# Kernel optimization log

Hardware: AMD Instinct MI355X
Metric: run time of the kernel (lower is better)

## Reference

```python
import jax, jax.numpy as jnp
import numpy as np

NEG = -1e10
EPS = 1e-5
H = 4  # num_heads


def layer_norm(y, g, b):
    m = jnp.mean(y, axis=-1, keepdims=True)
    v = jnp.mean((y - m) ** 2, axis=-1, keepdims=True)
    return (y - m) * jax.lax.rsqrt(v + EPS) * g + b


def setup_inputs() -> dict:
    key = jax.random.key(0)
    B, N, C = 16, 1024, 256
    ks = jax.random.split(key, 12)
    std = 0.1  # matches trunc_normal_(std=0.1) init
    inp = {
        "x": jax.random.normal(ks[0], (B, N, C), jnp.float32),
        "K": jax.random.normal(ks[1], (B, N, N), jnp.float32),
        "n1": jax.random.randint(ks[2], (B,), 8, 33),
        "n2": jax.random.randint(ks[3], (B,), 8, 33),
        "qkv_w": jax.random.normal(ks[4], (3 * C, C), jnp.float32) * std,
        "qkv_b": jnp.zeros((3 * C,), jnp.float32),
        "proj_w": jax.random.normal(ks[5], (C, C), jnp.float32) * std,
        "proj_b": jnp.zeros((C,), jnp.float32),
        "ln1_g": jnp.ones((C,), jnp.float32),
        "ln1_b": jnp.zeros((C,), jnp.float32),
        "ln2_g": jnp.ones((C,), jnp.float32),
        "ln2_b": jnp.zeros((C,), jnp.float32),
        "fc1_w": jax.random.normal(ks[6], (4 * C, C), jnp.float32) * std,
        "fc1_b": jnp.zeros((4 * C,), jnp.float32),
        "fc2_w": jax.random.normal(ks[7], (C, 4 * C), jnp.float32) * std,
        "fc2_b": jnp.zeros((C,), jnp.float32),
    }
    return inp


def reference(x, K, n1, n2, qkv_w, qkv_b, proj_w, proj_b,
              ln1_g, ln1_b, ln2_g, ln2_b, fc1_w, fc1_b, fc2_w, fc2_b):
    B, N, C = x.shape
    D = C // H
    scale = D ** -0.5

    # --- attention block ---
    h = layer_norm(x, ln1_g, ln1_b)
    qkv = (h @ qkv_w.T + qkv_b).reshape(B, N, 3, H, D)
    qkv = jnp.transpose(qkv, (2, 0, 3, 1, 4))  # [3,B,H,N,D]
    q, k, v = qkv[0], qkv[1], qkv[2]

    attn = jnp.einsum('bhnd,bhmd->bhnm', q, k) * scale  # [B,H,N,N]

    # per-sample dynamic block mask: rows>=n1*n2 fully masked; cols>=n1*n2 masked
    nrc = (n1 * n2)[:, None]                  # [B,1]
    invalid = jnp.arange(N)[None, :] >= nrc   # [B,N]
    mask = invalid[:, :, None] | invalid[:, None, :]  # [B,N,N]
    attn = jnp.where(mask[:, None], NEG, attn)
    attn = attn + K[:, None]                  # broadcast K over heads

    a = jax.nn.softmax(attn, axis=-1)
    o = jnp.einsum('bhnm,bhmd->bhnd', a, v)
    o = jnp.transpose(o, (0, 2, 1, 3)).reshape(B, N, C)
    x = x + (o @ proj_w.T + proj_b)

    # --- MLP block (exact GELU as torch nn.GELU) ---
    h2 = layer_norm(x, ln2_g, ln2_b)
    m = jax.nn.gelu(h2 @ fc1_w.T + fc1_b, approximate=False)
    m = m @ fc2_w.T + fc2_b
    return x + m
```

## Files before the change

### kernel.cpp

```cpp
#include <hip/hip_runtime.h>
#include <math.h>
#include <stdint.h>

constexpr int Bc = 16, Nn = 1024, Cc = 256, Hh = 4;
constexpr int Mrows = Bc * Nn;
constexpr float EPSV = 1e-5f;

typedef __attribute__((ext_vector_type(4))) float f32x4;
typedef __attribute__((ext_vector_type(8))) short bf16x8;

__device__ inline float wave_reduce_sum(float v) {
#pragma unroll
  for (int m = 32; m >= 1; m >>= 1) v += __shfl_xor(v, m);
  return v;
}

__device__ inline short f2bf(float f) {
  uint32_t u = __builtin_bit_cast(uint32_t, f);
  u = (u + 0x7fffu + ((u >> 16) & 1u)) >> 16;
  return (short)u;
}
__device__ inline float bf2f(short s) {
  uint32_t u = ((uint32_t)(uint16_t)s) << 16;
  return __builtin_bit_cast(float, u);
}

__device__ inline float gelu_fast(float x) {
  float x2 = x * x;
  float u = x * (0.7978845608028654f + 0.0356774081f * x2);
  float e = __builtin_amdgcn_exp2f(u * 2.8853900817779268f);
  return x * (1.f - __builtin_amdgcn_rcpf(e + 1.f));
}

#define GLDS(gptr, lptr)                                             \
  __builtin_amdgcn_global_load_lds(                                  \
      (const __attribute__((address_space(1))) void*)(gptr),         \
      (__attribute__((address_space(3))) void*)(lptr), 16, 0, 0)

__global__ __launch_bounds__(256)
void cvt_all(const float* __restrict__ s0, short* __restrict__ d0,
             const float* __restrict__ s1, short* __restrict__ d1,
             const float* __restrict__ s2, short* __restrict__ d2,
             const float* __restrict__ s3, short* __restrict__ d3) {
  int bid = blockIdx.x;
  const float* s;
  short* d;
  int base;
  if (bid < 192)      { s = s0; d = d0; base = bid; }
  else if (bid < 256) { s = s1; d = d1; base = bid - 192; }
  else if (bid < 512) { s = s2; d = d2; base = bid - 256; }
  else                { s = s3; d = d3; base = bid - 512; }
  int i = (base * 256 + threadIdx.x) * 4;
  float4 v = *(const float4*)(s + i);
  short4 o;
  o.x = f2bf(v.x); o.y = f2bf(v.y); o.z = f2bf(v.z); o.w = f2bf(v.w);
  *(short4*)(d + i) = o;
}

__global__ __launch_bounds__(256)
void ln_kernel(const float* __restrict__ x, const float* __restrict__ g,
               const float* __restrict__ b, short* __restrict__ h) {
  int row = blockIdx.x * 4 + (threadIdx.x >> 6);
  int lane = threadIdx.x & 63;
  const float4* xr = (const float4*)(x + (size_t)row * Cc);
  float4 v = xr[lane];
  float s = v.x + v.y + v.z + v.w;
  float sq = v.x * v.x + v.y * v.y + v.z * v.z + v.w * v.w;
  s = wave_reduce_sum(s);
  sq = wave_reduce_sum(sq);
  float mean = s * (1.f / Cc);
  float var = sq * (1.f / Cc) - mean * mean;
  float inv = rsqrtf(var + EPSV);
  float4 gg = ((const float4*)g)[lane];
  float4 bb = ((const float4*)b)[lane];
  short4 o;
  o.x = f2bf((v.x - mean) * inv * gg.x + bb.x);
  o.y = f2bf((v.y - mean) * inv * gg.y + bb.y);
  o.z = f2bf((v.z - mean) * inv * gg.z + bb.z);
  o.w = f2bf((v.w - mean) * inv * gg.w + bb.w);
  *(short4*)(h + (size_t)row * Cc + lane * 4) = o;
}

__global__ __launch_bounds__(256)
void qkv_mfma(const short* __restrict__ A, const short* __restrict__ Bw,
              const float* __restrict__ bias, short* __restrict__ qkp,
              short* __restrict__ vtp) {
  __shared__ __align__(16) short As[2][128 * 64];
  __shared__ __align__(16) short Bs[2][128 * 64];
  int t = threadIdx.x;
  int w = t >> 6, lane = t & 63;
  int wm = w >> 1, wn = w & 1;
  int l16 = lane & 15, lhi = lane >> 4;
  int m0 = blockIdx.y * 128, n0 = blockIdx.x * 128;
  const bool vblk = (n0 >= 512);
  f32x4 acc[4][4] = {};

#pragma unroll
  for (int i = 0; i < 4; ++i) {
    int cc = i * 256 + t;
    int r = cc >> 3, sl = cc & 7, ssl = sl ^ (r & 7);
    GLDS(A + (size_t)(m0 + r) * 256 + ssl * 8, &As[0][cc * 8]);
    GLDS(Bw + (size_t)(n0 + r) * 256 + ssl * 8, &Bs[0][cc * 8]);
  }

  int cur = 0;
  for (int k0 = 0; k0 < 256; k0 += 64, cur ^= 1) {
    asm volatile("s_waitcnt vmcnt(0)" ::: "memory");
    __syncthreads();
    int kn = k0 + 64;
    if (kn < 256) {
      int nxt = cur ^ 1;
#pragma unroll
      for (int i = 0; i < 4; ++i) {
        int cc = i * 256 + t;
        int r = cc >> 3, sl = cc & 7, ssl = sl ^ (r & 7);
        GLDS(A + (size_t)(m0 + r) * 256 + kn + ssl * 8, &As[nxt][cc * 8]);
        GLDS(Bw + (size_t)(n0 + r) * 256 + kn + ssl * 8, &Bs[nxt][cc * 8]);
      }
    }
#pragma unroll
    for (int ks = 0; ks < 2; ++ks) {
      bf16x8 af[4], bg[4];
#pragma unroll
      for (int mi = 0; mi < 4; ++mi) {
        int row = wm * 64 + mi * 16 + l16;
        af[mi] = *(const bf16x8*)&As[cur][row * 64 + ((ks * 32 + lhi * 8) ^ ((row & 7) << 3))];
      }
#pragma unroll
      for (int ni = 0; ni < 4; ++ni) {
        int row = wn * 64 + ni * 16 + l16;
        bg[ni] = *(const bf16x8*)&Bs[cur][row * 64 + ((ks * 32 + lhi * 8) ^ ((row & 7) << 3))];
      }
      if (!vblk) {
#pragma unroll
        for (int mi = 0; mi < 4; ++mi)
#pragma unroll
          for (int ni = 0; ni < 4; ++ni)
            acc[mi][ni] = __builtin_amdgcn_mfma_f32_16x16x32_bf16(
                af[mi], bg[ni], acc[mi][ni], 0, 0, 0);
      } else {
#pragma unroll
        for (int mi = 0; mi < 4; ++mi)
#pragma unroll
          for (int ni = 0; ni < 4; ++ni)
            acc[mi][ni] = __builtin_amdgcn_mfma_f32_16x16x32_bf16(
                bg[ni], af[mi], acc[mi][ni], 0, 0, 0);
      }
    }
  }

  if (!vblk) {
    const bool isq = (n0 < 256);
#pragma unroll
    for (int mi = 0; mi < 4; ++mi) {
      int mbase = m0 + wm * 64 + mi * 16 + lhi * 4;
#pragma unroll
      for (int ni = 0; ni < 4; ++ni) {
        int n = n0 + wn * 64 + ni * 16 + l16;
        int s = n >> 8, hh = (n >> 6) & 3, d = n & 63;
        float bv = bias[n];
#pragma unroll
        for (int r = 0; r < 4; ++r) {
          int m = mbase + r;
          int b = m >> 10, rw = m & 1023;
          float v = acc[mi][ni][r] + bv;
          if (isq) v *= 0.125f;
          qkp[(size_t)s * 4194304 + (((size_t)(b * 4 + hh)) * 1024 + rw) * 64 + d] = f2bf(v);
        }
      }
    }
  } else {
#pragma unroll
    for (int mi = 0; mi < 4; ++mi) {
#pragma unroll
      for (int ni = 0; ni < 4; ++ni) {
#pragma unroll
        for (int r = 0; r < 4; ++r) {
          int n = n0 + wn * 64 + ni * 16 + lhi * 4 + r;
          int hh = (n >> 6) & 3, d = n & 63;
          int m = m0 + wm * 64 + mi * 16 + l16;
          int b = m >> 10, rw = m & 1023;
          float v = acc[mi][ni][r] + bias[n];
          vtp[(((size_t)(b * 4 + hh)) * 64 + d) * 1024 + rw] = f2bf(v);
        }
      }
    }
  }
}

__global__ __launch_bounds__(256)
void vmean_kernel(const short* __restrict__ vt, short* __restrict__ vmb) {
  __shared__ float part[64][4];
  int bh = blockIdx.x;
  int d = threadIdx.x >> 2, seg = threadIdx.x & 3;
  const short* p = vt + (size_t)bh * 65536 + (size_t)d * 1024 + seg * 256;
  float s = 0.f;
  for (int i = 0; i < 256; i += 8) {
    bf16x8 v = *(const bf16x8*)(p + i);
#pragma unroll
    for (int j = 0; j < 8; ++j) s += bf2f(v[j]);
  }
  part[d][seg] = s;
  __syncthreads();
  if (threadIdx.x < 64) {
    int dd = threadIdx.x;
    float tot = part[dd][0] + part[dd][1] + part[dd][2] + part[dd][3];
    vmb[bh * 64 + dd] = f2bf(tot * (1.f / 1024.f));
  }
}

__global__ __launch_bounds__(256)
void fattn_mfma(const short* __restrict__ qpk, const short* __restrict__ kpk,
                const short* __restrict__ vt, const float* __restrict__ Kmat,
                const int* __restrict__ n1, const int* __restrict__ n2,
                const short* __restrict__ vmb, short* __restrict__ o,
                float* __restrict__ pO, float* __restrict__ pL,
                int tiles_per_split) {
  int bh = blockIdx.y, b = bh >> 2, hh = bh & 3;
  int qt = blockIdx.x;
  int row0 = qt * 64;
  int sp = blockIdx.z;
  int nc = n1[b] * n2[b];
  int t = threadIdx.x;
  __shared__ short vms[64];
  if (t < 64) vms[t] = vmb[bh * 64 + t];
  __syncthreads();
  if (row0 >= nc) {
    if (sp == 0) {
      for (int idx = t; idx < 4096; idx += 256) {
        int r = idx >> 6, d = idx & 63;
        o[((size_t)(b * 1024 + row0 + r)) * 256 + hh * 64 + d] = vms[d];
      }
    }
    return;
  }
  int ntiles = (nc + 63) >> 6;
  int nsp = (ntiles + tiles_per_split - 1) / tiles_per_split;
  int jt0 = sp * tiles_per_split;
  if (jt0 >= ntiles) return;
  int jstart = jt0 * 64;
  int jend = min(jstart + tiles_per_split * 64, nc);
  const bool final_out = (nsp == 1);

  __shared__ __align__(16) short Ks[2][64 * 64];
  __shared__ __align__(16) short Vs[2][64 * 64];
  __shared__ __align__(16) short Ps[64 * 64];
  int w = t >> 6, lane = t & 63, l16 = lane & 15, lhi = lane >> 4;

  constexpr float LOG2E = 1.4426950408889634f;
  constexpr float MREF = 12.0f;

  const short* qb = qpk + (size_t)bh * 65536 + (size_t)(row0 + w * 16 + l16) * 64;
  bf16x8 qf0 = *(const bf16x8*)(qb + lhi * 8);
  bf16x8 qf1 = *(const bf16x8*)(qb + 32 + lhi * 8);

  f32x4 accO[4] = {};
  float lsum[4] = {};
  const float* Kb = Kmat + (size_t)b * 1048576 + (size_t)(row0 + w * 16) * 1024;

  f32x4 kvp[4];

#pragma unroll
  for (int i = 0; i < 2; ++i) {
    int cc = i * 256 + t;
    int r = cc >> 3, sl = cc & 7, ssl = sl ^ (r & 7);
    GLDS(kpk + (size_t)bh * 65536 + (size_t)(jstart + r) * 64 + ssl * 8, &Ks[0][cc * 8]);
    GLDS(vt + (size_t)bh * 65536 + (size_t)r * 1024 + jstart + ssl * 8, &Vs[0][cc * 8]);
  }
#pragma unroll
  for (int ni = 0; ni < 4; ++ni)
#pragma unroll
    for (int r = 0; r < 4; ++r)
      kvp[ni][r] =
          (Kb[(size_t)(lhi * 4 + r) * 1024 + jstart + ni * 16 + l16] - MREF) * LOG2E;

  int cur = 0;
  for (int j0 = jstart; j0 < jend; j0 += 64, cur ^= 1) {
    asm volatile("s_waitcnt vmcnt(0)" ::: "memory");
    __syncthreads();

    f32x4 kvc[4];
#pragma unroll
    for (int i = 0; i < 4; ++i) kvc[i] = kvp[i];
    int jn = j0 + 64;
    if (jn < jend) {
      int nxt = cur ^ 1;
#pragma unroll
      for (int i = 0; i < 2; ++i) {
        int cc = i * 256 + t;
        int r = cc >> 3, sl = cc & 7, ssl = sl ^ (r & 7);
        GLDS(kpk + (size_t)bh * 65536 + (size_t)(jn + r) * 64 + ssl * 8, &Ks[nxt][cc * 8]);
        GLDS(vt + (size_t)bh * 65536 + (size_t)r * 1024 + jn + ssl * 8, &Vs[nxt][cc * 8]);
      }
#pragma unroll
      for (int ni = 0; ni < 4; ++ni)
#pragma unroll
        for (int r = 0; r < 4; ++r)
          kvp[ni][r] =
              (Kb[(size_t)(lhi * 4 + r) * 1024 + jn + ni * 16 + l16] - MREF) * LOG2E;
    }

    f32x4 accS[4] = {};
#pragma unroll
    for (int ks = 0; ks < 2; ++ks) {
#pragma unroll
      for (int ni = 0; ni < 4; ++ni) {
        int row = ni * 16 + l16;
        bf16x8 kf = *(const bf16x8*)&Ks[cur][row * 64 + (((ks * 4 + lhi) ^ (row & 7)) << 3)];
        accS[ni] = __builtin_amdgcn_mfma_f32_16x16x32_bf16(
            ks ? qf1 : qf0, kf, accS[ni], 0, 0, 0);
      }
    }

#pragma unroll
    for (int ni = 0; ni < 4; ++ni) {
      bool valid = (j0 + ni * 16 + l16) < nc;
#pragma unroll
      for (int r = 0; r < 4; ++r) {
        float e = __builtin_amdgcn_exp2f(fmaf(accS[ni][r], LOG2E, kvc[ni][r]));
        e = valid ? e : 0.f;
        lsum[r] += e;
        int prow = w * 16 + lhi * 4 + r;
        int col = ni * 16 + l16;
        Ps[prow * 64 + ((((col >> 3) ^ (prow & 7)) << 3) | (col & 7))] = f2bf(e);
      }
    }

#pragma unroll
    for (int ks = 0; ks < 2; ++ks) {
      int prow = w * 16 + l16;
      bf16x8 pf = *(const bf16x8*)&Ps[prow * 64 + (((ks * 4 + lhi) ^ (prow & 7)) << 3)];
#pragma unroll
      for (int ni = 0; ni < 4; ++ni) {
        int vrow = ni * 16 + l16;
        bf16x8 vf = *(const bf16x8*)&Vs[cur][vrow * 64 + (((ks * 4 + lhi) ^ (vrow & 7)) << 3)];
        accO[ni] = __builtin_amdgcn_mfma_f32_16x16x32_bf16(pf, vf, accO[ni], 0, 0, 0);
      }
    }
  }

#pragma unroll
  for (int r = 0; r < 4; ++r) {
    lsum[r] += __shfl_xor(lsum[r], 1);
    lsum[r] += __shfl_xor(lsum[r], 2);
    lsum[r] += __shfl_xor(lsum[r], 4);
    lsum[r] += __shfl_xor(lsum[r], 8);
  }

  if (final_out) {
#pragma unroll
    for (int ni = 0; ni < 4; ++ni) {
#pragma unroll
      for (int r = 0; r < 4; ++r) {
        int row = row0 + w * 16 + lhi * 4 + r;
        int d = ni * 16 + l16;
        short ov;
        if (row < nc) ov = f2bf(accO[ni][r] * (1.f / lsum[r]));
        else ov = vms[d];
        o[((size_t)(b * 1024 + row)) * 256 + hh * 64 + d] = ov;
      }
    }
  } else {
    float* po = pO + (((size_t)sp * 64 + bh) * 16 + qt) * 4096;
#pragma unroll
    for (int ni = 0; ni < 4; ++ni)
#pragma unroll
      for (int r = 0; r < 4; ++r)
        po[(w * 16 + lhi * 4 + r) * 64 + ni * 16 + l16] = accO[ni][r];
    if (l16 == 0) {
      float* pl = pL + (((size_t)sp * 64 + bh) * 16 + qt) * 64;
#pragma unroll
      for (int r = 0; r < 4; ++r) pl[w * 16 + lhi * 4 + r] = lsum[r];
    }
    if (sp == 0) {
      for (int idx = t; idx < 4096; idx += 256) {
        int r = idx >> 6, d = idx & 63;
        int row = row0 + r;
        if (row >= nc)
          o[((size_t)(b * 1024 + row)) * 256 + hh * 64 + d] = vms[d];
      }
    }
  }
}

__global__ __launch_bounds__(256)
void fattn_combine(const float* __restrict__ pO, const float* __restrict__ pL,
                   const int* __restrict__ n1, const int* __restrict__ n2,
                   short* __restrict__ o, int tiles_per_split) {
  int bh = blockIdx.y, b = bh >> 2, hh = bh & 3;
  int qt = blockIdx.x;
  int row0 = qt * 64;
  int nc = n1[b] * n2[b];
  if (row0 >= nc) return;
  int ntiles = (nc + 63) >> 6;
  int nsp = (ntiles + tiles_per_split - 1) / tiles_per_split;
  if (nsp < 2) return;

  int t = threadIdx.x;
  int q = t >> 2, ds = (t & 3) * 16;
  int row = row0 + q;
  if (row >= nc) return;

  const size_t spstrideO = (size_t)64 * 16 * 4096;
  const size_t spstrideL = (size_t)64 * 16 * 64;
  const float* baseO = pO + ((size_t)bh * 16 + qt) * 4096 + q * 64 + ds;
  const float* baseL = pL + ((size_t)bh * 16 + qt) * 64 + q;

  f32x4 s[4] = {};
  float L = 0.f;
  for (int sp = 0; sp < nsp; ++sp) {
    const float* p = baseO + sp * spstrideO;
#pragma unroll
    for (int i = 0; i < 4; ++i) s[i] += *(const f32x4*)(p + i * 4);
    L += baseL[sp * spstrideL];
  }
  float rl = 1.f / L;
  short* op = o + ((size_t)(b * 1024 + row)) * 256 + hh * 64 + ds;
#pragma unroll
  for (int i = 0; i < 4; ++i) {
    short4 ov;
    ov.x = f2bf(s[i][0] * rl);
    ov.y = f2bf(s[i][1] * rl);
    ov.z = f2bf(s[i][2] * rl);
    ov.w = f2bf(s[i][3] * rl);
    *(short4*)(op + i * 4) = ov;
  }
}

__global__ __launch_bounds__(256)
void proj_ln_mfma(const short* __restrict__ A, const short* __restrict__ Bw,
                  const float* __restrict__ bias, const float* __restrict__ resid,
                  const float* __restrict__ g2, const float* __restrict__ b2,
                  float* __restrict__ Cf, short* __restrict__ h2) {
  __shared__ __align__(16) short As[2][64 * 64];
  __shared__ __align__(16) short Bs[2][256 * 64];
  int t = threadIdx.x;
  int w = t >> 6, lane = t & 63;
  int l16 = lane & 15, lhi = lane >> 4;
  int m0 = blockIdx.x * 64;
  constexpr int Kd = 256;
  f32x4 acc[4][4] = {};

#pragma unroll
  for (int i = 0; i < 2; ++i) {
    int cc = i * 256 + t;
    int r = cc >> 3, sl = cc & 7, ssl = sl ^ (r & 7);
    GLDS(A + (size_t)(m0 + r) * Kd + ssl * 8, &As[0][cc * 8]);
  }
#pragma unroll
  for (int i = 0; i < 8; ++i) {
    int cc = i * 256 + t;
    int r = cc >> 3, sl = cc & 7, ssl = sl ^ (r & 7);
    GLDS(Bw + (size_t)r * Kd + ssl * 8, &Bs[0][cc * 8]);
  }

  int cur = 0;
  for (int k0 = 0; k0 < Kd; k0 += 64, cur ^= 1) {
    asm volatile("s_waitcnt vmcnt(0)" ::: "memory");
    __syncthreads();
    int kn = k0 + 64;
    if (kn < Kd) {
      int nxt = cur ^ 1;
#pragma unroll
      for (int i = 0; i < 2; ++i) {
        int cc = i * 256 + t;
        int r = cc >> 3, sl = cc & 7, ssl = sl ^ (r & 7);
        GLDS(A + (size_t)(m0 + r) * Kd + kn + ssl * 8, &As[nxt][cc * 8]);
      }
#pragma unroll
      for (int i = 0; i < 8; ++i) {
        int cc = i * 256 + t;
        int r = cc >> 3, sl = cc & 7, ssl = sl ^ (r & 7);
        GLDS(Bw + (size_t)r * Kd + kn + ssl * 8, &Bs[nxt][cc * 8]);
      }
    }
#pragma unroll
    for (int ks = 0; ks < 2; ++ks) {
      bf16x8 af[4], bg[4];
#pragma unroll
      for (int mi = 0; mi < 4; ++mi) {
        int row = mi * 16 + l16;
        af[mi] = *(const bf16x8*)&As[cur][row * 64 + ((ks * 32 + lhi * 8) ^ ((row & 7) << 3))];
      }
#pragma unroll
      for (int ni = 0; ni < 4; ++ni) {
        int row = w * 64 + ni * 16 + l16;
        bg[ni] = *(const bf16x8*)&Bs[cur][row * 64 + ((ks * 32 + lhi * 8) ^ ((row & 7) << 3))];
      }
#pragma unroll
      for (int mi = 0; mi < 4; ++mi)
#pragma unroll
        for (int ni = 0; ni < 4; ++ni)
          acc[mi][ni] = __builtin_amdgcn_mfma_f32_16x16x32_bf16(
              af[mi], bg[ni], acc[mi][ni], 0, 0, 0);
    }
  }

  float bv[4], gl[4], bl[4];
#pragma unroll
  for (int ni = 0; ni < 4; ++ni) {
    int n = w * 64 + ni * 16 + l16;
    bv[ni] = bias[n];
    gl[ni] = g2[n];
    bl[ni] = b2[n];
  }
#pragma unroll
  for (int mi = 0; mi < 4; ++mi)
#pragma unroll
    for (int ni = 0; ni < 4; ++ni) {
      int n = w * 64 + ni * 16 + l16;
#pragma unroll
      for (int r = 0; r < 4; ++r) {
        int m = m0 + mi * 16 + lhi * 4 + r;
        size_t idx = (size_t)m * 256 + n;
        float v = acc[mi][ni][r] + bv[ni] + resid[idx];
        acc[mi][ni][r] = v;
        Cf[idx] = v;
      }
    }

  float s[4][4], qq[4][4];
#pragma unroll
  for (int mi = 0; mi < 4; ++mi)
#pragma unroll
    for (int r = 0; r < 4; ++r) {
      float a0 = acc[mi][0][r], a1 = acc[mi][1][r];
      float a2 = acc[mi][2][r], a3 = acc[mi][3][r];
      s[mi][r] = a0 + a1 + a2 + a3;
      qq[mi][r] = a0 * a0 + a1 * a1 + a2 * a2 + a3 * a3;
    }
#pragma unroll
  for (int off = 1; off <= 8; off <<= 1)
#pragma unroll
    for (int mi = 0; mi < 4; ++mi)
#pragma unroll
      for (int r = 0; r < 4; ++r) {
        s[mi][r] += __shfl_xor(s[mi][r], off);
        qq[mi][r] += __shfl_xor(qq[mi][r], off);
      }

  __syncthreads();
  float* partS = (float*)&As[0][0];
  float* partQ = partS + 256;
  if (l16 == 0) {
#pragma unroll
    for (int mi = 0; mi < 4; ++mi)
#pragma unroll
      for (int r = 0; r < 4; ++r) {
        int row = mi * 16 + lhi * 4 + r;
        partS[w * 64 + row] = s[mi][r];
        partQ[w * 64 + row] = qq[mi][r];
      }
  }
  __syncthreads();

#pragma unroll
  for (int mi = 0; mi < 4; ++mi)
#pragma unroll
    for (int r = 0; r < 4; ++r) {
      int row = mi * 16 + lhi * 4 + r;
      float S = partS[row] + partS[64 + row] + partS[128 + row] + partS[192 + row];
      float Q = partQ[row] + partQ[64 + row] + partQ[128 + row] + partQ[192 + row];
      float mean = S * (1.f / 256.f);
      float var = Q * (1.f / 256.f) - mean * mean;
      float inv = rsqrtf(var + EPSV);
      int m = m0 + row;
#pragma unroll
      for (int ni = 0; ni < 4; ++ni) {
        int n = w * 64 + ni * 16 + l16;
        h2[(size_t)m * 256 + n] =
            f2bf((acc[mi][ni][r] - mean) * inv * gl[ni] + bl[ni]);
      }
    }
}

template <bool GELU, bool RES, bool OUTF, bool OUTB>
__global__ __launch_bounds__(256)
void gemm_mfma(const short* __restrict__ A, const short* __restrict__ Bw,
               const float* __restrict__ bias, const float* __restrict__ resid,
               float* __restrict__ Cf, short* __restrict__ Cb,
               int M, int Nd, int Kd) {
  __shared__ __align__(16) short As[2][128 * 64];
  __shared__ __align__(16) short Bs[2][128 * 64];
  int t = threadIdx.x;
  int w = t >> 6, lane = t & 63;
  int wm = w >> 1, wn = w & 1;
  int l16 = lane & 15, lhi = lane >> 4;
  int m0 = blockIdx.y * 128, n0 = blockIdx.x * 128;
  f32x4 acc[4][4] = {};

#pragma unroll
  for (int i = 0; i < 4; ++i) {
    int cc = i * 256 + t;
    int r = cc >> 3, sl = cc & 7, ssl = sl ^ (r & 7);
    GLDS(A + (size_t)(m0 + r) * Kd + ssl * 8, &As[0][cc * 8]);
    GLDS(Bw + (size_t)(n0 + r) * Kd + ssl * 8, &Bs[0][cc * 8]);
  }

  int cur = 0;
  for (int k0 = 0; k0 < Kd; k0 += 64, cur ^= 1) {
    asm volatile("s_waitcnt vmcnt(0)" ::: "memory");
    __syncthreads();
    int kn = k0 + 64;
    if (kn < Kd) {
      int nxt = cur ^ 1;
#pragma unroll
      for (int i = 0; i < 4; ++i) {
        int cc = i * 256 + t;
        int r = cc >> 3, sl = cc & 7, ssl = sl ^ (r & 7);
        GLDS(A + (size_t)(m0 + r) * Kd + kn + ssl * 8, &As[nxt][cc * 8]);
        GLDS(Bw + (size_t)(n0 + r) * Kd + kn + ssl * 8, &Bs[nxt][cc * 8]);
      }
    }
#pragma unroll
    for (int ks = 0; ks < 2; ++ks) {
      bf16x8 af[4], bg[4];
#pragma unroll
      for (int mi = 0; mi < 4; ++mi) {
        int row = wm * 64 + mi * 16 + l16;
        af[mi] = *(const bf16x8*)&As[cur][row * 64 + ((ks * 32 + lhi * 8) ^ ((row & 7) << 3))];
      }
#pragma unroll
      for (int ni = 0; ni < 4; ++ni) {
        int row = wn * 64 + ni * 16 + l16;
        bg[ni] = *(const bf16x8*)&Bs[cur][row * 64 + ((ks * 32 + lhi * 8) ^ ((row & 7) << 3))];
      }
#pragma unroll
      for (int mi = 0; mi < 4; ++mi)
#pragma unroll
        for (int ni = 0; ni < 4; ++ni)
          acc[mi][ni] = __builtin_amdgcn_mfma_f32_16x16x32_bf16(
              af[mi], bg[ni], acc[mi][ni], 0, 0, 0);
    }
  }
#pragma unroll
  for (int mi = 0; mi < 4; ++mi) {
    int rbase = m0 + wm * 64 + mi * 16 + lhi * 4;
#pragma unroll
    for (int ni = 0; ni < 4; ++ni) {
      int n = n0 + wn * 64 + ni * 16 + l16;
      float bv = bias[n];
#pragma unroll
      for (int r = 0; r < 4; ++r) {
        int m = rbase + r;
        float v = acc[mi][ni][r] + bv;
        if (GELU) v = gelu_fast(v);
        size_t idx = (size_t)m * Nd + n;
        if (RES) v += resid[idx];
        if (OUTF) Cf[idx] = v;
        if (OUTB) Cb[idx] = f2bf(v);
      }
    }
  }
}

template <bool GELU, bool RES, bool OUTF, bool OUTB>
__global__ __launch_bounds__(256)
void gemm64_mfma(const short* __restrict__ A, const short* __restrict__ Bw,
                 const float* __restrict__ bias, const float* __restrict__ resid,
                 float* __restrict__ Cf, short* __restrict__ Cb,
                 int M, int Nd, int Kd) {
  __shared__ __align__(16) short As[2][64 * 64];
  __shared__ __align__(16) short Bs[2][128 * 64];
  int t = threadIdx.x;
  int w = t >> 6, lane = t & 63;
  int l16 = lane & 15, lhi = lane >> 4;
  int m0 = blockIdx.y * 64, n0 = blockIdx.x * 128;
  f32x4 acc[4][2] = {};

#pragma unroll
  for (int i = 0; i < 2; ++i) {
    int cc = i * 256 + t;
    int r = cc >> 3, sl = cc & 7, ssl = sl ^ (r & 7);
    GLDS(A + (size_t)(m0 + r) * Kd + ssl * 8, &As[0][cc * 8]);
  }
#pragma unroll
  for (int i = 0; i < 4; ++i) {
    int cc = i * 256 + t;
    int r = cc >> 3, sl = cc & 7, ssl = sl ^ (r & 7);
    GLDS(Bw + (size_t)(n0 + r) * Kd + ssl * 8, &Bs[0][cc * 8]);
  }

  int cur = 0;
  for (int k0 = 0; k0 < Kd; k0 += 64, cur ^= 1) {
    asm volatile("s_waitcnt vmcnt(0)" ::: "memory");
    __syncthreads();
    int kn = k0 + 64;
    if (kn < Kd) {
      int nxt = cur ^ 1;
#pragma unroll
      for (int i = 0; i < 2; ++i) {
        int cc = i * 256 + t;
        int r = cc >> 3, sl = cc & 7, ssl = sl ^ (r & 7);
        GLDS(A + (size_t)(m0 + r) * Kd + kn + ssl * 8, &As[nxt][cc * 8]);
      }
#pragma unroll
      for (int i = 0; i < 4; ++i) {
        int cc = i * 256 + t;
        int r = cc >> 3, sl = cc & 7, ssl = sl ^ (r & 7);
        GLDS(Bw + (size_t)(n0 + r) * Kd + kn + ssl * 8, &Bs[nxt][cc * 8]);
      }
    }
#pragma unroll
    for (int ks = 0; ks < 2; ++ks) {
      bf16x8 af[4], bg[2];
#pragma unroll
      for (int mi = 0; mi < 4; ++mi) {
        int row = mi * 16 + l16;
        af[mi] = *(const bf16x8*)&As[cur][row * 64 + ((ks * 32 + lhi * 8) ^ ((row & 7) << 3))];
      }
#pragma unroll
      for (int ni = 0; ni < 2; ++ni) {
        int row = w * 32 + ni * 16 + l16;
        bg[ni] = *(const bf16x8*)&Bs[cur][row * 64 + ((ks * 32 + lhi * 8) ^ ((row & 7) << 3))];
      }
#pragma unroll
      for (int mi = 0; mi < 4; ++mi)
#pragma unroll
        for (int ni = 0; ni < 2; ++ni)
          acc[mi][ni] = __builtin_amdgcn_mfma_f32_16x16x32_bf16(
              af[mi], bg[ni], acc[mi][ni], 0, 0, 0);
    }
  }
#pragma unroll
  for (int mi = 0; mi < 4; ++mi) {
    int rbase = m0 + mi * 16 + lhi * 4;
#pragma unroll
    for (int ni = 0; ni < 2; ++ni) {
      int n = n0 + w * 32 + ni * 16 + l16;
      float bv = bias[n];
#pragma unroll
      for (int r = 0; r < 4; ++r) {
        int m = rbase + r;
        float v = acc[mi][ni][r] + bv;
        if (GELU) v = gelu_fast(v);
        size_t idx = (size_t)m * Nd + n;
        if (RES) v += resid[idx];
        if (OUTF) Cf[idx] = v;
        if (OUTB) Cb[idx] = f2bf(v);
      }
    }
  }
}

extern "C" void kernel_launch(void* const* d_in, const int* in_sizes, int n_in,
                              void* d_out, int out_size, void* d_ws, size_t ws_size,
                              hipStream_t stream) {
  const float* x      = (const float*)d_in[0];
  const float* Kmat   = (const float*)d_in[1];
  const int*   n1     = (const int*)d_in[2];
  const int*   n2     = (const int*)d_in[3];
  const float* qkv_w  = (const float*)d_in[4];
  const float* qkv_b  = (const float*)d_in[5];
  const float* proj_w = (const float*)d_in[6];
  const float* proj_b = (const float*)d_in[7];
  const float* ln1_g  = (const float*)d_in[8];
  const float* ln1_b  = (const float*)d_in[9];
  const float* ln2_g  = (const float*)d_in[10];
  const float* ln2_b  = (const float*)d_in[11];
  const float* fc1_w  = (const float*)d_in[12];
  const float* fc1_b  = (const float*)d_in[13];
  const float* fc2_w  = (const float*)d_in[14];
  const float* fc2_b  = (const float*)d_in[15];
  float* out = (float*)d_out;

  char* ws = (char*)d_ws;
  constexpr size_t MB = 1024 * 1024;
  short* hb    = (short*)ws;
  short* qkp   = (short*)(ws + 8 * MB);
  short* vtp   = (short*)(ws + 24 * MB);
  short* m1    = (short*)(ws + 8 * MB);
  short* vmb   = (short*)(ws + 40 * MB);
  short* wqkv  = (short*)(ws + 41 * MB);
  short* wproj = (short*)(ws + 42 * MB);
  short* wfc1  = (short*)(ws + 43 * MB);
  short* wfc2  = (short*)(ws + 44 * MB);
  float* pO    = (float*)(ws + 48 * MB);
  float* pL    = (float*)(ws + 116 * MB);
  short* hb2   = (short*)(ws + 48 * MB);
  short* obuf  = hb;
  short* qpk   = qkp;
  short* kpk   = qkp + 4194304;

  const bool split = ws_size >= (size_t)118 * MB;

  cvt_all<<<dim3(768), 256, 0, stream>>>(qkv_w, wqkv, proj_w, wproj,
                                         fc1_w, wfc1, fc2_w, wfc2);
  ln_kernel<<<dim3(Mrows / 4), 256, 0, stream>>>(x, ln1_g, ln1_b, hb);
  qkv_mfma<<<dim3(6, 128), 256, 0, stream>>>(hb, wqkv, qkv_b, qkp, vtp);
  vmean_kernel<<<dim3(Bc * Hh), 256, 0, stream>>>(vtp, vmb);
  if (split) {
    fattn_mfma<<<dim3(Nn / 64, Bc * Hh, 4), 256, 0, stream>>>(
        qpk, kpk, vtp, Kmat, n1, n2, vmb, obuf, pO, pL, 4);
    fattn_combine<<<dim3(Nn / 64, Bc * Hh), 256, 0, stream>>>(
        pO, pL, n1, n2, obuf, 4);
  } else {
    fattn_mfma<<<dim3(Nn / 64, Bc * Hh, 1), 256, 0, stream>>>(
        qpk, kpk, vtp, Kmat, n1, n2, vmb, obuf, pO, pL, 16);
  }
  proj_ln_mfma<<<dim3(256), 256, 0, stream>>>(
      obuf, wproj, proj_b, x, ln2_g, ln2_b, out, hb2);
  gemm_mfma<true, false, false, true><<<dim3(8, 128), 256, 0, stream>>>(
      hb2, wfc1, fc1_b, nullptr, nullptr, m1, Mrows, 1024, 256);
  gemm64_mfma<false, true, true, false><<<dim3(2, 256), 256, 0, stream>>>(
      m1, wfc2, fc2_b, out, out, nullptr, Mrows, 256, 1024);
}
```

Before: 131.8 us.

## Widen attention key tile to 128 columns and defer K-bias prefetch

```diff
diff --git a/kernel.cpp b/kernel.cpp
--- a/kernel.cpp
+++ b/kernel.cpp
@@ -222,29 +222,26 @@
   int sp = blockIdx.z;
   int nc = n1[b] * n2[b];
   int t = threadIdx.x;
-  __shared__ short vms[64];
-  if (t < 64) vms[t] = vmb[bh * 64 + t];
-  __syncthreads();
   if (row0 >= nc) {
     if (sp == 0) {
       for (int idx = t; idx < 4096; idx += 256) {
         int r = idx >> 6, d = idx & 63;
-        o[((size_t)(b * 1024 + row0 + r)) * 256 + hh * 64 + d] = vms[d];
+        o[((size_t)(b * 1024 + row0 + r)) * 256 + hh * 64 + d] = vmb[bh * 64 + d];
       }
     }
     return;
   }
-  int ntiles = (nc + 63) >> 6;
+  int ntiles = (nc + 127) >> 7;
   int nsp = (ntiles + tiles_per_split - 1) / tiles_per_split;
   int jt0 = sp * tiles_per_split;
   if (jt0 >= ntiles) return;
-  int jstart = jt0 * 64;
-  int jend = min(jstart + tiles_per_split * 64, nc);
+  int jstart = jt0 * 128;
+  int jend = min(jstart + tiles_per_split * 128, nc);
   const bool final_out = (nsp == 1);
 
-  __shared__ __align__(16) short Ks[2][64 * 64];
-  __shared__ __align__(16) short Vs[2][64 * 64];
-  __shared__ __align__(16) short Ps[64 * 64];
+  __shared__ __align__(16) short Ks[2][128 * 64];
+  __shared__ __align__(16) short Vs[2][64 * 128];
+  __shared__ __align__(16) short Ps[64 * 128];
   int w = t >> 6, lane = t & 63, l16 = lane & 15, lhi = lane >> 4;
 
   constexpr float LOG2E = 1.4426950408889634f;
@@ -258,53 +255,46 @@
   float lsum[4] = {};
   const float* Kb = Kmat + (size_t)b * 1048576 + (size_t)(row0 + w * 16) * 1024;
 
-  f32x4 kvp[4];
-
-#pragma unroll
-  for (int i = 0; i < 2; ++i) {
+  f32x4 kvp[8];
+
+#pragma unroll
+  for (int i = 0; i < 4; ++i) {
     int cc = i * 256 + t;
-    int r = cc >> 3, sl = cc & 7, ssl = sl ^ (r & 7);
-    GLDS(kpk + (size_t)bh * 65536 + (size_t)(jstart + r) * 64 + ssl * 8, &Ks[0][cc * 8]);
-    GLDS(vt + (size_t)bh * 65536 + (size_t)r * 1024 + jstart + ssl * 8, &Vs[0][cc * 8]);
-  }
-#pragma unroll
-  for (int ni = 0; ni < 4; ++ni)
+    int rk = cc >> 3, slk = cc & 7, sslk = slk ^ (rk & 7);
+    GLDS(kpk + (size_t)bh * 65536 + (size_t)(jstart + rk) * 64 + sslk * 8, &Ks[0][cc * 8]);
+    int rv = cc >> 4, slv = cc & 15, sslv = slv ^ (rv & 7);
+    GLDS(vt + (size_t)bh * 65536 + (size_t)rv * 1024 + jstart + sslv * 8, &Vs[0][cc * 8]);
+  }
+#pragma unroll
+  for (int ni = 0; ni < 8; ++ni)
 #pragma unroll
     for (int r = 0; r < 4; ++r)
       kvp[ni][r] =
           (Kb[(size_t)(lhi * 4 + r) * 1024 + jstart + ni * 16 + l16] - MREF) * LOG2E;
 
   int cur = 0;
-  for (int j0 = jstart; j0 < jend; j0 += 64, cur ^= 1) {
+  for (int j0 = jstart; j0 < jend; j0 += 128, cur ^= 1) {
     asm volatile("s_waitcnt vmcnt(0)" ::: "memory");
     __syncthreads();
 
-    f32x4 kvc[4];
-#pragma unroll
-    for (int i = 0; i < 4; ++i) kvc[i] = kvp[i];
-    int jn = j0 + 64;
+    int jn = j0 + 128;
     if (jn < jend) {
       int nxt = cur ^ 1;
 #pragma unroll
-      for (int i = 0; i < 2; ++i) {
+      for (int i = 0; i < 4; ++i) {
         int cc = i * 256 + t;
-        int r = cc >> 3, sl = cc & 7, ssl = sl ^ (r & 7);
-        GLDS(kpk + (size_t)bh * 65536 + (size_t)(jn + r) * 64 + ssl * 8, &Ks[nxt][cc * 8]);
-        GLDS(vt + (size_t)bh * 65536 + (size_t)r * 1024 + jn + ssl * 8, &Vs[nxt][cc * 8]);
-      }
-#pragma unroll
-      for (int ni = 0; ni < 4; ++ni)
-#pragma unroll
-        for (int r = 0; r < 4; ++r)
-          kvp[ni][r] =
-              (Kb[(size_t)(lhi * 4 + r) * 1024 + jn + ni * 16 + l16] - MREF) * LOG2E;
-    }
-
-    f32x4 accS[4] = {};
+        int rk = cc >> 3, slk = cc & 7, sslk = slk ^ (rk & 7);
+        GLDS(kpk + (size_t)bh * 65536 + (size_t)(jn + rk) * 64 + sslk * 8, &Ks[nxt][cc * 8]);
+        int rv = cc >> 4, slv = cc & 15, sslv = slv ^ (rv & 7);
+        GLDS(vt + (size_t)bh * 65536 + (size_t)rv * 1024 + jn + sslv * 8, &Vs[nxt][cc * 8]);
+      }
+    }
+
+    f32x4 accS[8] = {};
 #pragma unroll
     for (int ks = 0; ks < 2; ++ks) {
 #pragma unroll
-      for (int ni = 0; ni < 4; ++ni) {
+      for (int ni = 0; ni < 8; ++ni) {
         int row = ni * 16 + l16;
         bf16x8 kf = *(const bf16x8*)&Ks[cur][row * 64 + (((ks * 4 + lhi) ^ (row & 7)) << 3)];
         accS[ni] = __builtin_amdgcn_mfma_f32_16x16x32_bf16(
@@ -313,27 +303,36 @@
     }
 
 #pragma unroll
-    for (int ni = 0; ni < 4; ++ni) {
+    for (int ni = 0; ni < 8; ++ni) {
       bool valid = (j0 + ni * 16 + l16) < nc;
+      int col16 = ni * 16 + l16;
 #pragma unroll
       for (int r = 0; r < 4; ++r) {
-        float e = __builtin_amdgcn_exp2f(fmaf(accS[ni][r], LOG2E, kvc[ni][r]));
+        float e = __builtin_amdgcn_exp2f(fmaf(accS[ni][r], LOG2E, kvp[ni][r]));
         e = valid ? e : 0.f;
         lsum[r] += e;
         int prow = w * 16 + lhi * 4 + r;
-        int col = ni * 16 + l16;
-        Ps[prow * 64 + ((((col >> 3) ^ (prow & 7)) << 3) | (col & 7))] = f2bf(e);
-      }
-    }
-
-#pragma unroll
-    for (int ks = 0; ks < 2; ++ks) {
+        Ps[prow * 128 + ((((col16 >> 3) ^ (prow & 7)) << 3) | (col16 & 7))] = f2bf(e);
+      }
+    }
+
+    if (jn < jend) {
+#pragma unroll
+      for (int ni = 0; ni < 8; ++ni)
+#pragma unroll
+        for (int r = 0; r < 4; ++r)
+          kvp[ni][r] =
+              (Kb[(size_t)(lhi * 4 + r) * 1024 + jn + ni * 16 + l16] - MREF) * LOG2E;
+    }
+
+#pragma unroll
+    for (int ks = 0; ks < 4; ++ks) {
       int prow = w * 16 + l16;
-      bf16x8 pf = *(const bf16x8*)&Ps[prow * 64 + (((ks * 4 + lhi) ^ (prow & 7)) << 3)];
+      bf16x8 pf = *(const bf16x8*)&Ps[prow * 128 + (((ks * 4 + lhi) ^ (prow & 7)) << 3)];
 #pragma unroll
       for (int ni = 0; ni < 4; ++ni) {
         int vrow = ni * 16 + l16;
-        bf16x8 vf = *(const bf16x8*)&Vs[cur][vrow * 64 + (((ks * 4 + lhi) ^ (vrow & 7)) << 3)];
+        bf16x8 vf = *(const bf16x8*)&Vs[cur][vrow * 128 + (((ks * 4 + lhi) ^ (vrow & 7)) << 3)];
         accO[ni] = __builtin_amdgcn_mfma_f32_16x16x32_bf16(pf, vf, accO[ni], 0, 0, 0);
       }
     }
@@ -356,7 +355,7 @@
         int d = ni * 16 + l16;
         short ov;
         if (row < nc) ov = f2bf(accO[ni][r] * (1.f / lsum[r]));
-        else ov = vms[d];
+        else ov = vmb[bh * 64 + d];
         o[((size_t)(b * 1024 + row)) * 256 + hh * 64 + d] = ov;
       }
     }
@@ -377,7 +376,7 @@
         int r = idx >> 6, d = idx & 63;
         int row = row0 + r;
         if (row >= nc)
-          o[((size_t)(b * 1024 + row)) * 256 + hh * 64 + d] = vms[d];
+          o[((size_t)(b * 1024 + row)) * 256 + hh * 64 + d] = vmb[bh * 64 + d];
       }
     }
   }
@@ -392,7 +391,7 @@
   int row0 = qt * 64;
   int nc = n1[b] * n2[b];
   if (row0 >= nc) return;
-  int ntiles = (nc + 63) >> 6;
+  int ntiles = (nc + 127) >> 7;
   int nsp = (ntiles + tiles_per_split - 1) / tiles_per_split;
   if (nsp < 2) return;
 
@@ -791,12 +790,12 @@
   vmean_kernel<<<dim3(Bc * Hh), 256, 0, stream>>>(vtp, vmb);
   if (split) {
     fattn_mfma<<<dim3(Nn / 64, Bc * Hh, 4), 256, 0, stream>>>(
-        qpk, kpk, vtp, Kmat, n1, n2, vmb, obuf, pO, pL, 4);
+        qpk, kpk, vtp, Kmat, n1, n2, vmb, obuf, pO, pL, 2);
     fattn_combine<<<dim3(Nn / 64, Bc * Hh), 256, 0, stream>>>(
-        pO, pL, n1, n2, obuf, 4);
+        pO, pL, n1, n2, obuf, 2);
   } else {
     fattn_mfma<<<dim3(Nn / 64, Bc * Hh, 1), 256, 0, stream>>>(
-        qpk, kpk, vtp, Kmat, n1, n2, vmb, obuf, pO, pL, 16);
+        qpk, kpk, vtp, Kmat, n1, n2, vmb, obuf, pO, pL, 8);
   }
   proj_ln_mfma<<<dim3(256), 256, 0, stream>>>(
       obuf, wproj, proj_b, x, ln2_g, ln2_b, out, hb2);
```

Result: slower. 136.4 us (+3.5%).
